# Optimization experiments

Hardware: AMD Instinct MI355X
Metric: run time of the kernel (lower is better)

The kernel has to match this reference:

```python
import jax, jax.numpy as jnp
import numpy as np

N_EMBD = 1024
N_HEAD = 16
B, T = 2, 2048


def setup_inputs() -> dict:
    key = jax.random.key(0)
    ks = jax.random.split(key, 9)
    s = 1.0 / np.sqrt(N_EMBD)
    return {
        "x": jax.random.normal(ks[0], (B, T, N_EMBD), dtype=jnp.float32),
        "Wq": jax.random.normal(ks[1], (N_EMBD, N_EMBD), dtype=jnp.float32) * s,
        "bq": jax.random.normal(ks[2], (N_EMBD,), dtype=jnp.float32) * s,
        "Wk": jax.random.normal(ks[3], (N_EMBD, N_EMBD), dtype=jnp.float32) * s,
        "bk": jax.random.normal(ks[4], (N_EMBD,), dtype=jnp.float32) * s,
        "Wv": jax.random.normal(ks[5], (N_EMBD, N_EMBD), dtype=jnp.float32) * s,
        "bv": jax.random.normal(ks[6], (N_EMBD,), dtype=jnp.float32) * s,
        "Wp": jax.random.normal(ks[7], (N_EMBD, N_EMBD), dtype=jnp.float32) * s,
        "bp": jax.random.normal(ks[8], (N_EMBD,), dtype=jnp.float32) * s,
    }


def reference(x, Wq, bq, Wk, bk, Wv, bv, Wp, bp):
    b, t, c = x.shape
    hd = c // N_HEAD  # head dim
    # torch Linear: x @ W.T + b; reshape to (B, H, T, hd)
    def heads(W, bias):
        return (x @ W.T + bias).reshape(b, t, N_HEAD, hd).transpose(0, 2, 1, 3)
    q, k, v = heads(Wq, bq), heads(Wk, bk), heads(Wv, bv)
    scale = 1.0 / np.sqrt(hd)
    att = jnp.einsum("bhqd,bhkd->bhqk", q, k) * scale  # (B,H,T,T)
    causal = jnp.tril(jnp.ones((t, t), dtype=bool))
    att = jnp.where(causal[None, None], att, -jnp.inf)
    att = jax.nn.softmax(att, axis=-1)
    y = jnp.einsum("bhqk,bhkd->bhqd", att, v)
    y = y.transpose(0, 2, 1, 3).reshape(b, t, c)
    return y @ Wp.T + bp
```

## Files before the change

kernel.cpp:

```cpp
#include <hip/hip_runtime.h>

typedef __bf16 bf16x8 __attribute__((ext_vector_type(8)));
typedef __bf16 bf16x4 __attribute__((ext_vector_type(4)));
typedef float f32x4 __attribute__((ext_vector_type(4)));

#define DEVI __device__ __forceinline__

constexpr int NE = 1024;
constexpr int NH = 16;
constexpr int HD = 64;
constexpr int BB = 2;
constexpr int TT = 2048;
constexpr int MM = BB * TT;

DEVI unsigned short f2bf(float f) {
  union { float f; unsigned u; } v; v.f = f;
  unsigned r = v.u + 0x7FFFu + ((v.u >> 16) & 1u);
  return (unsigned short)(r >> 16);
}

__global__ __launch_bounds__(256) void cvt_bf16(const float* __restrict__ in,
                                                unsigned short* __restrict__ out, int n4) {
  int i = blockIdx.x * blockDim.x + threadIdx.x;
  if (i >= n4) return;
  float4 v = reinterpret_cast<const float4*>(in)[i];
  ushort4 o;
  o.x = f2bf(v.x); o.y = f2bf(v.y); o.z = f2bf(v.z); o.w = f2bf(v.w);
  reinterpret_cast<ushort4*>(out)[i] = o;
}

__global__ __launch_bounds__(256) void cvt_w(const float* __restrict__ q, const float* __restrict__ k,
                                             const float* __restrict__ v, const float* __restrict__ p,
                                             unsigned short* __restrict__ out) {
  int i = blockIdx.x * blockDim.x + threadIdx.x;
  const int seg = i >> 18;
  const float* src = (seg == 0) ? q : (seg == 1) ? k : (seg == 2) ? v : p;
  float4 vv = reinterpret_cast<const float4*>(src)[i & 0x3FFFF];
  ushort4 o;
  o.x = f2bf(vv.x); o.y = f2bf(vv.y); o.z = f2bf(vv.z); o.w = f2bf(vv.w);
  reinterpret_cast<ushort4*>(out)[i] = o;
}

template <int BM, int MODE>
__global__ __launch_bounds__(256, (BM == 128) ? 3 : 2)
void gemm_nt(const unsigned short* __restrict__ A, const unsigned short* __restrict__ Bm,
             const float* __restrict__ b0, const float* __restrict__ b1, const float* __restrict__ b2,
             void* __restrict__ o0, unsigned short* __restrict__ o1, unsigned short* __restrict__ o2,
             int K, int nbx) {
  constexpr int WAVES_N = (BM == 128) ? 2 : 4;
  constexpr int NJ = (BM == 128) ? 4 : 2;
  constexpr int A_LPW = BM / 64;
  __shared__ __align__(16) unsigned short As[3][BM * 32];
  __shared__ __align__(16) unsigned short Bs[3][128 * 32];
  const int tid = threadIdx.x;
  const int wid = tid >> 6;
  const int lane = tid & 63;
  const int l15 = lane & 15, l4 = lane >> 4;

  const int id = blockIdx.x;
  const int chunk = gridDim.x >> 3;
  const int idp = (id & 7) * chunk + (id >> 3);
  const int bx = idp / (gridDim.x / nbx), by = idp % (gridDim.x / nbx);

  const int brow = by * BM;
  const int bcol = bx * 128;
  const int wm = wid / WAVES_N, wn = wid % WAVES_N;
  const int wmoff = wm * 64;
  const int wnoff = wn * (128 / WAVES_N);

  f32x4 acc[4][NJ] = {};

  const int srow = lane >> 2;
  const int sscol = ((lane & 3) ^ ((lane >> 3) & 3)) * 8;

  auto stage = [&](int buf, int t) {
    const int kb = t * 32;
#pragma unroll
    for (int c = 0; c < A_LPW; ++c) {
      const int rb = wid * (BM / 4) + c * 16;
      __builtin_amdgcn_global_load_lds(
          (const __attribute__((address_space(1))) void*)(A + (size_t)(brow + rb + srow) * K + kb + sscol),
          (__attribute__((address_space(3))) void*)&As[buf][rb * 32], 16, 0, 0);
    }
#pragma unroll
    for (int c = 0; c < 2; ++c) {
      const int rb = wid * 32 + c * 16;
      __builtin_amdgcn_global_load_lds(
          (const __attribute__((address_space(1))) void*)(Bm + (size_t)(bcol + rb + srow) * K + kb + sscol),
          (__attribute__((address_space(3))) void*)&Bs[buf][rb * 32], 16, 0, 0);
    }
  };

  const int roff = l15 * 32 + (l4 ^ ((l15 >> 1) & 3)) * 8;

  auto compute = [&](int cb) {
    bf16x8 af[4], bfj[NJ];
#pragma unroll
    for (int i = 0; i < 4; ++i)
      af[i] = *reinterpret_cast<const bf16x8*>(&As[cb][(wmoff + i * 16) * 32 + roff]);
#pragma unroll
    for (int j = 0; j < NJ; ++j)
      bfj[j] = *reinterpret_cast<const bf16x8*>(&Bs[cb][(wnoff + j * 16) * 32 + roff]);
#pragma unroll
    for (int i = 0; i < 4; ++i)
#pragma unroll
      for (int j = 0; j < NJ; ++j)
        acc[i][j] = __builtin_amdgcn_mfma_f32_16x16x32_bf16(af[i], bfj[j], acc[i][j], 0, 0, 0);
  };

  const int NT = K / 32;
  stage(0, 0);
  stage(1, 1);
  int cb = 0, sb = 2;
  for (int t = 0; t + 2 < NT; ++t) {
    stage(sb, t + 2);
    if constexpr (BM == 128) asm volatile("s_waitcnt vmcnt(8)" ::: "memory");
    else                     asm volatile("s_waitcnt vmcnt(6)" ::: "memory");
    asm volatile("s_barrier" ::: "memory");
    compute(cb);
    asm volatile("s_barrier" ::: "memory");
    sb = cb;
    cb = (cb == 2) ? 0 : cb + 1;
  }
  if constexpr (BM == 128) asm volatile("s_waitcnt vmcnt(4)" ::: "memory");
  else                     asm volatile("s_waitcnt vmcnt(3)" ::: "memory");
  asm volatile("s_barrier" ::: "memory");
  compute(cb);
  asm volatile("s_barrier" ::: "memory");
  cb = (cb == 2) ? 0 : cb + 1;
  asm volatile("s_waitcnt vmcnt(0)" ::: "memory");
  asm volatile("s_barrier" ::: "memory");
  compute(cb);

  if (MODE == 0) {
#pragma unroll
    for (int j = 0; j < NJ; ++j) {
      const int col = bcol + wnoff + j * 16 + l15;
      const float bv = b0[col];
#pragma unroll
      for (int i = 0; i < 4; ++i) {
        const int row0 = brow + wmoff + i * 16 + l4 * 4;
#pragma unroll
        for (int r = 0; r < 4; ++r)
          ((float*)o0)[(size_t)(row0 + r) * NE + col] = acc[i][j][r] + bv;
      }
    }
  } else {
    const int seg = bcol >> 10;
    const float* bsel = (seg == 0) ? b0 : (seg == 1) ? b1 : b2;
    unsigned short* qk = (seg == 0) ? (unsigned short*)o0 : o1;
#pragma unroll
    for (int j = 0; j < NJ; ++j) {
      const int col = bcol + wnoff + j * 16 + l15;
      const int dcol = col & 1023;
      const int h = dcol >> 6, d = dcol & 63;
      const float bv = bsel[dcol];
#pragma unroll
      for (int i = 0; i < 4; ++i) {
        const int row0 = brow + wmoff + i * 16 + l4 * 4;
#pragma unroll
        for (int r = 0; r < 4; ++r) {
          const int row = row0 + r;
          const int b = row >> 11, t = row & (TT - 1);
          const unsigned short val = f2bf(acc[i][j][r] + bv);
          if (seg < 2)
            qk[((size_t)((b * NH + h) * TT + t) << 6) + d] = val;
          else
            o2[((size_t)(b * NH + h) * HD + d) * TT + t] = val;
        }
      }
    }
  }
}

__global__ __launch_bounds__(256, 3)
void attn(const unsigned short* __restrict__ Q, const unsigned short* __restrict__ Kk,
          const unsigned short* __restrict__ Vt, unsigned short* __restrict__ Y) {
  __shared__ __align__(16) unsigned short Ks[2][64 * 64];
  __shared__ __align__(16) unsigned short Vs[2][64 * 64];
  __shared__ __align__(16) unsigned short Pw[4][32 * 64];
  const int tid = threadIdx.x, wid = tid >> 6, lane = tid & 63;
  const int l15 = lane & 15, l4 = lane >> 4;

  const int id = blockIdx.x;
  const int v8 = id & 7;
  const int u = id >> 3;
  const int bh = u >> 1;
  const int xt = (u & 1) ? 15 - v8 : v8;

  const int qb0 = xt * 128;
  const int qw = qb0 + wid * 32;
  const unsigned short* Qh = Q + (size_t)bh * TT * HD;
  const unsigned short* Kh = Kk + (size_t)bh * TT * HD;
  const unsigned short* Vh = Vt + (size_t)bh * HD * TT;

  bf16x8 qf[2][2];
#pragma unroll
  for (int qt = 0; qt < 2; ++qt)
#pragma unroll
    for (int ks = 0; ks < 2; ++ks) {
      bf16x8 t = *reinterpret_cast<const bf16x8*>(&Qh[(qw + qt * 16 + l15) * 64 + ks * 32 + l4 * 8]);
#pragma unroll
      for (int e = 0; e < 8; ++e) t[e] = (__bf16)((float)t[e] * 0.18033688011f);
      qf[qt][ks] = t;
    }

  float m_[2] = {-3e38f, -3e38f};
  float l_[2] = {0.f, 0.f};
  f32x4 accO[4][2] = {};

  const int srow8 = lane >> 3;
  const int scol8 = lane & 7;
  const int nkb = 2 * (xt + 1);

  auto stage = [&](int buf, int kb) {
#pragma unroll
    for (int c = 0; c < 2; ++c) {
      const int row = (wid * 2 + c) * 8 + srow8;
      const int sc = (scol8 ^ (row & 7)) * 8;
      __builtin_amdgcn_global_load_lds(
          (const __attribute__((address_space(1))) void*)(Kh + (size_t)(kb + row) * 64 + sc),
          (__attribute__((address_space(3))) void*)&Ks[buf][(wid * 2 + c) * 512], 16, 0, 0);
      __builtin_amdgcn_global_load_lds(
          (const __attribute__((address_space(1))) void*)(Vh + (size_t)row * TT + kb + sc),
          (__attribute__((address_space(3))) void*)&Vs[buf][(wid * 2 + c) * 512], 16, 0, 0);
    }
  };

  stage(0, 0);
  int cur = 0;
  for (int kbi = 0; kbi < nkb; ++kbi) {
    const int kb = kbi * 64;
    __syncthreads();
    if (kbi + 1 < nkb) stage(cur ^ 1, kb + 64);

    if (kb < qw + 32) {
      const bool diag = (kb + 63 > qw);
      const char* ksb = (const char*)Ks[cur];
      const char* vsb = (const char*)Vs[cur];
      char* pwb = (char*)&Pw[wid][0];

      f32x4 z[4][2];
      __builtin_amdgcn_s_setprio(1);
#pragma unroll
      for (int kt = 0; kt < 4; ++kt) {
        const int row = kt * 16 + l15;
        bf16x8 kf0 = *reinterpret_cast<const bf16x8*>(ksb + row * 128 + (((0 + l4) ^ (row & 7)) << 4));
        bf16x8 kf1 = *reinterpret_cast<const bf16x8*>(ksb + row * 128 + (((4 + l4) ^ (row & 7)) << 4));
#pragma unroll
        for (int qt = 0; qt < 2; ++qt) {
          f32x4 zz = {};
          zz = __builtin_amdgcn_mfma_f32_16x16x32_bf16(kf0, qf[qt][0], zz, 0, 0, 0);
          zz = __builtin_amdgcn_mfma_f32_16x16x32_bf16(kf1, qf[qt][1], zz, 0, 0, 0);
          z[kt][qt] = zz;
        }
      }
      __builtin_amdgcn_s_setprio(0);

      if (diag) {
#pragma unroll
        for (int kt = 0; kt < 4; ++kt)
#pragma unroll
          for (int qt = 0; qt < 2; ++qt)
#pragma unroll
            for (int r = 0; r < 4; ++r) {
              const int key = kb + kt * 16 + l4 * 4 + r;
              const int qi = qw + qt * 16 + l15;
              z[kt][qt][r] = (key <= qi) ? z[kt][qt][r] : -3e38f;
            }
      }

#pragma unroll
      for (int qt = 0; qt < 2; ++qt) {
        float tm[8];
#pragma unroll
        for (int i = 0; i < 8; ++i)
          tm[i] = fmaxf(z[(2 * i) >> 2][qt][(2 * i) & 3], z[(2 * i + 1) >> 2][qt][(2 * i + 1) & 3]);
#pragma unroll
        for (int i = 0; i < 4; ++i) tm[i] = fmaxf(tm[i], tm[i + 4]);
        float pm = fmaxf(fmaxf(tm[0], tm[2]), fmaxf(tm[1], tm[3]));
        pm = fmaxf(pm, __shfl_xor(pm, 16, 64));
        pm = fmaxf(pm, __shfl_xor(pm, 32, 64));

        if (!__all(pm <= m_[qt] + 11.5f)) {
          const float mn = fmaxf(m_[qt], pm);
          const float sf = exp2f(m_[qt] - mn);
          m_[qt] = mn;
          l_[qt] *= sf;
#pragma unroll
          for (int dt = 0; dt < 4; ++dt)
#pragma unroll
            for (int r = 0; r < 4; ++r) accO[dt][qt][r] *= sf;
        }

#pragma unroll
        for (int kt = 0; kt < 4; ++kt)
#pragma unroll
          for (int r = 0; r < 4; ++r)
            z[kt][qt][r] = exp2f(z[kt][qt][r] - m_[qt]);
        float ts[8];
#pragma unroll
        for (int i = 0; i < 8; ++i)
          ts[i] = z[(2 * i) >> 2][qt][(2 * i) & 3] + z[(2 * i + 1) >> 2][qt][(2 * i + 1) & 3];
#pragma unroll
        for (int i = 0; i < 4; ++i) ts[i] += ts[i + 4];
        float rs = (ts[0] + ts[2]) + (ts[1] + ts[3]);
        rs += __shfl_xor(rs, 16, 64);
        rs += __shfl_xor(rs, 32, 64);
        l_[qt] += rs;

        const int q = qt * 16 + l15;
#pragma unroll
        for (int kt = 0; kt < 4; ++kt) {
          bf16x4 pk;
#pragma unroll
          for (int r = 0; r < 4; ++r) pk[r] = (__bf16)z[kt][qt][r];
          const int c16 = kt * 2 + (l4 >> 1);
          *reinterpret_cast<bf16x4*>(pwb + q * 128 + ((c16 ^ (q & 7)) << 4) + (l4 & 1) * 8) = pk;
        }
      }

      asm volatile("s_waitcnt lgkmcnt(0)" ::: "memory");
      __builtin_amdgcn_sched_barrier(0);

      __builtin_amdgcn_s_setprio(1);
#pragma unroll
      for (int ks = 0; ks < 2; ++ks) {
        bf16x8 pb[2];
#pragma unroll
        for (int qt = 0; qt < 2; ++qt) {
          const int q = qt * 16 + l15;
          pb[qt] = *reinterpret_cast<const bf16x8*>(pwb + q * 128 + ((((ks << 2) + l4) ^ (q & 7)) << 4));
        }
#pragma unroll
        for (int dt = 0; dt < 4; ++dt) {
          const int row = dt * 16 + l15;
          bf16x8 vf = *reinterpret_cast<const bf16x8*>(vsb + row * 128 + ((((ks << 2) + l4) ^ (row & 7)) << 4));
#pragma unroll
          for (int qt = 0; qt < 2; ++qt)
            accO[dt][qt] = __builtin_amdgcn_mfma_f32_16x16x32_bf16(vf, pb[qt], accO[dt][qt], 0, 0, 0);
        }
      }
      __builtin_amdgcn_s_setprio(0);
    }
    cur ^= 1;
  }

  const int b = bh >> 4, h = bh & 15;
#pragma unroll
  for (int qt = 0; qt < 2; ++qt) {
    const float inv = 1.0f / l_[qt];
    const int q = qw + qt * 16 + l15;
#pragma unroll
    for (int dt = 0; dt < 4; ++dt) {
      bf16x4 o;
#pragma unroll
      for (int r = 0; r < 4; ++r) o[r] = (__bf16)(accO[dt][qt][r] * inv);
      *reinterpret_cast<bf16x4*>(&Y[((size_t)(b * TT + q)) * NE + h * 64 + dt * 16 + l4 * 4]) = o;
    }
  }
}

extern "C" void kernel_launch(void* const* d_in, const int* in_sizes, int n_in,
                              void* d_out, int out_size, void* d_ws, size_t ws_size,
                              hipStream_t stream) {
  const float* x  = (const float*)d_in[0];
  const float* Wq = (const float*)d_in[1];
  const float* bq = (const float*)d_in[2];
  const float* Wk = (const float*)d_in[3];
  const float* bk = (const float*)d_in[4];
  const float* Wv = (const float*)d_in[5];
  const float* bv = (const float*)d_in[6];
  const float* Wp = (const float*)d_in[7];
  const float* bp = (const float*)d_in[8];

  char* ws = (char*)d_ws;
  const size_t MB = 1u << 20;
  unsigned short* xb   = (unsigned short*)(ws + 0 * MB);
  unsigned short* Wqkv = (unsigned short*)(ws + 8 * MB);
  unsigned short* Wpb  = (unsigned short*)(ws + 14 * MB);
  unsigned short* Qb   = (unsigned short*)(ws + 16 * MB);
  unsigned short* Kb   = (unsigned short*)(ws + 24 * MB);
  unsigned short* Vtb  = (unsigned short*)(ws + 32 * MB);
  unsigned short* yb   = (unsigned short*)(ws + 40 * MB);

  cvt_bf16<<<MM * NE / 4 / 256, 256, 0, stream>>>(x, xb, MM * NE / 4);
  cvt_w<<<4 * NE * NE / 4 / 256, 256, 0, stream>>>(Wq, Wk, Wv, Wp, Wqkv);

  gemm_nt<128, 1><<<768, 256, 0, stream>>>(xb, Wqkv, bq, bk, bv, Qb, Kb, Vtb, NE, 24);

  attn<<<512, 256, 0, stream>>>(Qb, Kb, Vtb, yb);

  gemm_nt<64, 0><<<512, 256, 0, stream>>>(yb, Wpb, bp, nullptr, nullptr, d_out, nullptr, nullptr, NE, 8);
}
```

Baseline: 239.6 us.

## Triple-buffer K/V tiles in attention with vmcnt-based waits and reorder block mapping

Moves the attention kernel from double to triple buffering of K/V tiles in LDS. Two tiles are staged ahead, and explicit s_waitcnt vmcnt plus raw s_barrier replace __syncthreads, so global loads overlap more compute. The block-to-(batch-head, q-tile) mapping is also changed so co-scheduled blocks mix different heads and causal lengths. The extra LDS and the lowered occupancy hint (3 to 2 blocks per CU) reduce resident waves, and the hand-counted vmcnt values must match the per-thread load count.

```diff
diff --git a/kernel.cpp b/kernel.cpp
--- a/kernel.cpp
+++ b/kernel.cpp
@@ -173,20 +173,19 @@
   }
 }
 
-__global__ __launch_bounds__(256, 3)
+__global__ __launch_bounds__(256, 2)
 void attn(const unsigned short* __restrict__ Q, const unsigned short* __restrict__ Kk,
           const unsigned short* __restrict__ Vt, unsigned short* __restrict__ Y) {
-  __shared__ __align__(16) unsigned short Ks[2][64 * 64];
-  __shared__ __align__(16) unsigned short Vs[2][64 * 64];
+  __shared__ __align__(16) unsigned short Ks[3][64 * 64];
+  __shared__ __align__(16) unsigned short Vs[3][64 * 64];
   __shared__ __align__(16) unsigned short Pw[4][32 * 64];
   const int tid = threadIdx.x, wid = tid >> 6, lane = tid & 63;
   const int l15 = lane & 15, l4 = lane >> 4;
 
   const int id = blockIdx.x;
-  const int v8 = id & 7;
-  const int u = id >> 3;
-  const int bh = u >> 1;
-  const int xt = (u & 1) ? 15 - v8 : v8;
+  const int j = id & 255, kk = id >> 8;
+  const int bh = (j & 15) + 16 * kk;
+  const int xt = kk ? 15 - (j >> 4) : (j >> 4);
 
   const int qb0 = xt * 128;
   const int qw = qb0 + wid * 32;
@@ -227,124 +226,134 @@
     }
   };
 
+  auto compute_iter = [&](int kbi, int buf) {
+    const int kb = kbi * 64;
+    if (kb >= qw + 32) return;
+    const bool diag = (kb + 63 > qw);
+    const char* ksb = (const char*)Ks[buf];
+    const char* vsb = (const char*)Vs[buf];
+    char* pwb = (char*)&Pw[wid][0];
+
+    f32x4 z[4][2];
+    __builtin_amdgcn_s_setprio(1);
+#pragma unroll
+    for (int kt = 0; kt < 4; ++kt) {
+      const int row = kt * 16 + l15;
+      bf16x8 kf0 = *reinterpret_cast<const bf16x8*>(ksb + row * 128 + (((0 + l4) ^ (row & 7)) << 4));
+      bf16x8 kf1 = *reinterpret_cast<const bf16x8*>(ksb + row * 128 + (((4 + l4) ^ (row & 7)) << 4));
+#pragma unroll
+      for (int qt = 0; qt < 2; ++qt) {
+        f32x4 zz = {};
+        zz = __builtin_amdgcn_mfma_f32_16x16x32_bf16(kf0, qf[qt][0], zz, 0, 0, 0);
+        zz = __builtin_amdgcn_mfma_f32_16x16x32_bf16(kf1, qf[qt][1], zz, 0, 0, 0);
+        z[kt][qt] = zz;
+      }
+    }
+    __builtin_amdgcn_s_setprio(0);
+
+    if (diag) {
+#pragma unroll
+      for (int kt = 0; kt < 4; ++kt)
+#pragma unroll
+        for (int qt = 0; qt < 2; ++qt)
+#pragma unroll
+          for (int r = 0; r < 4; ++r) {
+            const int key = kb + kt * 16 + l4 * 4 + r;
+            const int qi = qw + qt * 16 + l15;
+            z[kt][qt][r] = (key <= qi) ? z[kt][qt][r] : -3e38f;
+          }
+    }
+
+#pragma unroll
+    for (int qt = 0; qt < 2; ++qt) {
+      float tm[8];
+#pragma unroll
+      for (int i = 0; i < 8; ++i)
+        tm[i] = fmaxf(z[(2 * i) >> 2][qt][(2 * i) & 3], z[(2 * i + 1) >> 2][qt][(2 * i + 1) & 3]);
+#pragma unroll
+      for (int i = 0; i < 4; ++i) tm[i] = fmaxf(tm[i], tm[i + 4]);
+      float pm = fmaxf(fmaxf(tm[0], tm[2]), fmaxf(tm[1], tm[3]));
+      pm = fmaxf(pm, __shfl_xor(pm, 16, 64));
+      pm = fmaxf(pm, __shfl_xor(pm, 32, 64));
+
+      if (!__all(pm <= m_[qt] + 11.5f)) {
+        const float mn = fmaxf(m_[qt], pm);
+        const float sf = exp2f(m_[qt] - mn);
+        m_[qt] = mn;
+        l_[qt] *= sf;
+#pragma unroll
+        for (int dt = 0; dt < 4; ++dt)
+#pragma unroll
+          for (int r = 0; r < 4; ++r) accO[dt][qt][r] *= sf;
+      }
+
+#pragma unroll
+      for (int kt = 0; kt < 4; ++kt)
+#pragma unroll
+        for (int r = 0; r < 4; ++r)
+          z[kt][qt][r] = exp2f(z[kt][qt][r] - m_[qt]);
+      float ts[8];
+#pragma unroll
+      for (int i = 0; i < 8; ++i)
+        ts[i] = z[(2 * i) >> 2][qt][(2 * i) & 3] + z[(2 * i + 1) >> 2][qt][(2 * i + 1) & 3];
+#pragma unroll
+      for (int i = 0; i < 4; ++i) ts[i] += ts[i + 4];
+      float rs = (ts[0] + ts[2]) + (ts[1] + ts[3]);
+      rs += __shfl_xor(rs, 16, 64);
+      rs += __shfl_xor(rs, 32, 64);
+      l_[qt] += rs;
+
+      const int q = qt * 16 + l15;
+#pragma unroll
+      for (int kt = 0; kt < 4; ++kt) {
+        bf16x4 pk;
+#pragma unroll
+        for (int r = 0; r < 4; ++r) pk[r] = (__bf16)z[kt][qt][r];
+        const int c16 = kt * 2 + (l4 >> 1);
+        *reinterpret_cast<bf16x4*>(pwb + q * 128 + ((c16 ^ (q & 7)) << 4) + (l4 & 1) * 8) = pk;
+      }
+    }
+
+    asm volatile("s_waitcnt lgkmcnt(0)" ::: "memory");
+    __builtin_amdgcn_sched_barrier(0);
+
+    __builtin_amdgcn_s_setprio(1);
+#pragma unroll
+    for (int ks = 0; ks < 2; ++ks) {
+      bf16x8 pb[2];
+#pragma unroll
+      for (int qt = 0; qt < 2; ++qt) {
+        const int q = qt * 16 + l15;
+        pb[qt] = *reinterpret_cast<const bf16x8*>(pwb + q * 128 + ((((ks << 2) + l4) ^ (q & 7)) << 4));
+      }
+#pragma unroll
+      for (int dt = 0; dt < 4; ++dt) {
+        const int row = dt * 16 + l15;
+        bf16x8 vf = *reinterpret_cast<const bf16x8*>(vsb + row * 128 + ((((ks << 2) + l4) ^ (row & 7)) << 4));
+#pragma unroll
+        for (int qt = 0; qt < 2; ++qt)
+          accO[dt][qt] = __builtin_amdgcn_mfma_f32_16x16x32_bf16(vf, pb[qt], accO[dt][qt], 0, 0, 0);
+      }
+    }
+    __builtin_amdgcn_s_setprio(0);
+  };
+
   stage(0, 0);
-  int cur = 0;
-  for (int kbi = 0; kbi < nkb; ++kbi) {
-    const int kb = kbi * 64;
-    __syncthreads();
-    if (kbi + 1 < nkb) stage(cur ^ 1, kb + 64);
-
-    if (kb < qw + 32) {
-      const bool diag = (kb + 63 > qw);
-      const char* ksb = (const char*)Ks[cur];
-      const char* vsb = (const char*)Vs[cur];
-      char* pwb = (char*)&Pw[wid][0];
-
-      f32x4 z[4][2];
-      __builtin_amdgcn_s_setprio(1);
-#pragma unroll
-      for (int kt = 0; kt < 4; ++kt) {
-        const int row = kt * 16 + l15;
-        bf16x8 kf0 = *reinterpret_cast<const bf16x8*>(ksb + row * 128 + (((0 + l4) ^ (row & 7)) << 4));
-        bf16x8 kf1 = *reinterpret_cast<const bf16x8*>(ksb + row * 128 + (((4 + l4) ^ (row & 7)) << 4));
-#pragma unroll
-        for (int qt = 0; qt < 2; ++qt) {
-          f32x4 zz = {};
-          zz = __builtin_amdgcn_mfma_f32_16x16x32_bf16(kf0, qf[qt][0], zz, 0, 0, 0);
-          zz = __builtin_amdgcn_mfma_f32_16x16x32_bf16(kf1, qf[qt][1], zz, 0, 0, 0);
-          z[kt][qt] = zz;
-        }
-      }
-      __builtin_amdgcn_s_setprio(0);
-
-      if (diag) {
-#pragma unroll
-        for (int kt = 0; kt < 4; ++kt)
-#pragma unroll
-          for (int qt = 0; qt < 2; ++qt)
-#pragma unroll
-            for (int r = 0; r < 4; ++r) {
-              const int key = kb + kt * 16 + l4 * 4 + r;
-              const int qi = qw + qt * 16 + l15;
-              z[kt][qt][r] = (key <= qi) ? z[kt][qt][r] : -3e38f;
-            }
-      }
-
-#pragma unroll
-      for (int qt = 0; qt < 2; ++qt) {
-        float tm[8];
-#pragma unroll
-        for (int i = 0; i < 8; ++i)
-          tm[i] = fmaxf(z[(2 * i) >> 2][qt][(2 * i) & 3], z[(2 * i + 1) >> 2][qt][(2 * i + 1) & 3]);
-#pragma unroll
-        for (int i = 0; i < 4; ++i) tm[i] = fmaxf(tm[i], tm[i + 4]);
-        float pm = fmaxf(fmaxf(tm[0], tm[2]), fmaxf(tm[1], tm[3]));
-        pm = fmaxf(pm, __shfl_xor(pm, 16, 64));
-        pm = fmaxf(pm, __shfl_xor(pm, 32, 64));
-
-        if (!__all(pm <= m_[qt] + 11.5f)) {
-          const float mn = fmaxf(m_[qt], pm);
-          const float sf = exp2f(m_[qt] - mn);
-          m_[qt] = mn;
-          l_[qt] *= sf;
-#pragma unroll
-          for (int dt = 0; dt < 4; ++dt)
-#pragma unroll
-            for (int r = 0; r < 4; ++r) accO[dt][qt][r] *= sf;
-        }
-
-#pragma unroll
-        for (int kt = 0; kt < 4; ++kt)
-#pragma unroll
-          for (int r = 0; r < 4; ++r)
-            z[kt][qt][r] = exp2f(z[kt][qt][r] - m_[qt]);
-        float ts[8];
-#pragma unroll
-        for (int i = 0; i < 8; ++i)
-          ts[i] = z[(2 * i) >> 2][qt][(2 * i) & 3] + z[(2 * i + 1) >> 2][qt][(2 * i + 1) & 3];
-#pragma unroll
-        for (int i = 0; i < 4; ++i) ts[i] += ts[i + 4];
-        float rs = (ts[0] + ts[2]) + (ts[1] + ts[3]);
-        rs += __shfl_xor(rs, 16, 64);
-        rs += __shfl_xor(rs, 32, 64);
-        l_[qt] += rs;
-
-        const int q = qt * 16 + l15;
-#pragma unroll
-        for (int kt = 0; kt < 4; ++kt) {
-          bf16x4 pk;
-#pragma unroll
-          for (int r = 0; r < 4; ++r) pk[r] = (__bf16)z[kt][qt][r];
-          const int c16 = kt * 2 + (l4 >> 1);
-          *reinterpret_cast<bf16x4*>(pwb + q * 128 + ((c16 ^ (q & 7)) << 4) + (l4 & 1) * 8) = pk;
-        }
-      }
-
-      asm volatile("s_waitcnt lgkmcnt(0)" ::: "memory");
-      __builtin_amdgcn_sched_barrier(0);
-
-      __builtin_amdgcn_s_setprio(1);
-#pragma unroll
-      for (int ks = 0; ks < 2; ++ks) {
-        bf16x8 pb[2];
-#pragma unroll
-        for (int qt = 0; qt < 2; ++qt) {
-          const int q = qt * 16 + l15;
-          pb[qt] = *reinterpret_cast<const bf16x8*>(pwb + q * 128 + ((((ks << 2) + l4) ^ (q & 7)) << 4));
-        }
-#pragma unroll
-        for (int dt = 0; dt < 4; ++dt) {
-          const int row = dt * 16 + l15;
-          bf16x8 vf = *reinterpret_cast<const bf16x8*>(vsb + row * 128 + ((((ks << 2) + l4) ^ (row & 7)) << 4));
-#pragma unroll
-          for (int qt = 0; qt < 2; ++qt)
-            accO[dt][qt] = __builtin_amdgcn_mfma_f32_16x16x32_bf16(vf, pb[qt], accO[dt][qt], 0, 0, 0);
-        }
-      }
-      __builtin_amdgcn_s_setprio(0);
-    }
-    cur ^= 1;
+  stage(1, 64);
+  for (int t = 0; t + 2 < nkb; ++t) {
+    stage((t + 2) % 3, (t + 2) * 64);
+    asm volatile("s_waitcnt vmcnt(8)" ::: "memory");
+    asm volatile("s_barrier" ::: "memory");
+    compute_iter(t, t % 3);
+    asm volatile("s_barrier" ::: "memory");
   }
+  asm volatile("s_waitcnt vmcnt(4)" ::: "memory");
+  asm volatile("s_barrier" ::: "memory");
+  compute_iter(nkb - 2, (nkb - 2) % 3);
+  asm volatile("s_barrier" ::: "memory");
+  asm volatile("s_waitcnt vmcnt(0)" ::: "memory");
+  asm volatile("s_barrier" ::: "memory");
+  compute_iter(nkb - 1, (nkb - 1) % 3);
 
   const int b = bh >> 4, h = bh & 15;
 #pragma unroll
```

New measurement: 223.6 us. -6.7%, faster.

## Widen attention key tile to 128 and remap blocks across heads

Applied to the files above, without the earlier changes.

The attention kernel now processes 128 keys per iteration instead of 64, with larger double-buffered K/V shared tiles and a new XOR swizzle for the wider V tile. This halves the loop trip count, syncs and online-softmax rescale checks per key. It also removes the per-wave skip branch, since the last tile is always the diagonal one. Block-index mapping changes so the first half of the grid walks query tiles ascending and the second half descending across heads, to balance causal work. The cost is doubled shared memory and more live registers, so launch bounds drop to 2 blocks per CU, reducing occupancy.

```diff
diff --git a/kernel.cpp b/kernel.cpp
--- a/kernel.cpp
+++ b/kernel.cpp
@@ -173,23 +173,22 @@
   }
 }
 
-__global__ __launch_bounds__(256, 3)
+__global__ __launch_bounds__(256, 2)
 void attn(const unsigned short* __restrict__ Q, const unsigned short* __restrict__ Kk,
           const unsigned short* __restrict__ Vt, unsigned short* __restrict__ Y) {
-  __shared__ __align__(16) unsigned short Ks[2][64 * 64];
-  __shared__ __align__(16) unsigned short Vs[2][64 * 64];
+  __shared__ __align__(16) unsigned short Ks[2][128 * 64];
+  __shared__ __align__(16) unsigned short Vs[2][64 * 128];
   __shared__ __align__(16) unsigned short Pw[4][32 * 64];
   const int tid = threadIdx.x, wid = tid >> 6, lane = tid & 63;
   const int l15 = lane & 15, l4 = lane >> 4;
 
   const int id = blockIdx.x;
-  const int v8 = id & 7;
-  const int u = id >> 3;
-  const int bh = u >> 1;
-  const int xt = (u & 1) ? 15 - v8 : v8;
-
-  const int qb0 = xt * 128;
-  const int qw = qb0 + wid * 32;
+  const int j = id & 255, kk = id >> 8;
+  const int bh = (j & 15) + 16 * kk;
+  const int xt = kk ? 15 - (j >> 4) : (j >> 4);
+
+  const int qw = xt * 128 + wid * 32;
+  const int nkb = xt + 1;
   const unsigned short* Qh = Q + (size_t)bh * TT * HD;
   const unsigned short* Kh = Kk + (size_t)bh * TT * HD;
   const unsigned short* Vh = Vt + (size_t)bh * HD * TT;
@@ -209,139 +208,151 @@
   float l_[2] = {0.f, 0.f};
   f32x4 accO[4][2] = {};
 
-  const int srow8 = lane >> 3;
-  const int scol8 = lane & 7;
-  const int nkb = 2 * (xt + 1);
-
   auto stage = [&](int buf, int kb) {
 #pragma unroll
-    for (int c = 0; c < 2; ++c) {
-      const int row = (wid * 2 + c) * 8 + srow8;
-      const int sc = (scol8 ^ (row & 7)) * 8;
+    for (int c = 0; c < 4; ++c) {
+      const int row = wid * 32 + c * 8 + (lane >> 3);
+      const int sc = ((lane & 7) ^ (lane >> 3)) * 8;
       __builtin_amdgcn_global_load_lds(
           (const __attribute__((address_space(1))) void*)(Kh + (size_t)(kb + row) * 64 + sc),
-          (__attribute__((address_space(3))) void*)&Ks[buf][(wid * 2 + c) * 512], 16, 0, 0);
+          (__attribute__((address_space(3))) void*)&Ks[buf][(wid * 32 + c * 8) * 64], 16, 0, 0);
+    }
+#pragma unroll
+    for (int c = 0; c < 4; ++c) {
+      const int row = wid * 16 + c * 4 + (lane >> 4);
+      const int sc = ((lane & 15) ^ (c * 4 + (lane >> 4))) * 8;
       __builtin_amdgcn_global_load_lds(
           (const __attribute__((address_space(1))) void*)(Vh + (size_t)row * TT + kb + sc),
-          (__attribute__((address_space(3))) void*)&Vs[buf][(wid * 2 + c) * 512], 16, 0, 0);
+          (__attribute__((address_space(3))) void*)&Vs[buf][(wid * 16 + c * 4) * 128], 16, 0, 0);
     }
   };
 
   stage(0, 0);
   int cur = 0;
   for (int kbi = 0; kbi < nkb; ++kbi) {
-    const int kb = kbi * 64;
+    const int kb = kbi * 128;
     __syncthreads();
-    if (kbi + 1 < nkb) stage(cur ^ 1, kb + 64);
-
-    if (kb < qw + 32) {
-      const bool diag = (kb + 63 > qw);
-      const char* ksb = (const char*)Ks[cur];
-      const char* vsb = (const char*)Vs[cur];
-      char* pwb = (char*)&Pw[wid][0];
-
-      f32x4 z[4][2];
-      __builtin_amdgcn_s_setprio(1);
-#pragma unroll
-      for (int kt = 0; kt < 4; ++kt) {
-        const int row = kt * 16 + l15;
-        bf16x8 kf0 = *reinterpret_cast<const bf16x8*>(ksb + row * 128 + (((0 + l4) ^ (row & 7)) << 4));
-        bf16x8 kf1 = *reinterpret_cast<const bf16x8*>(ksb + row * 128 + (((4 + l4) ^ (row & 7)) << 4));
-#pragma unroll
-        for (int qt = 0; qt < 2; ++qt) {
-          f32x4 zz = {};
-          zz = __builtin_amdgcn_mfma_f32_16x16x32_bf16(kf0, qf[qt][0], zz, 0, 0, 0);
-          zz = __builtin_amdgcn_mfma_f32_16x16x32_bf16(kf1, qf[qt][1], zz, 0, 0, 0);
-          z[kt][qt] = zz;
-        }
-      }
-      __builtin_amdgcn_s_setprio(0);
-
-      if (diag) {
-#pragma unroll
-        for (int kt = 0; kt < 4; ++kt)
-#pragma unroll
-          for (int qt = 0; qt < 2; ++qt)
-#pragma unroll
-            for (int r = 0; r < 4; ++r) {
-              const int key = kb + kt * 16 + l4 * 4 + r;
-              const int qi = qw + qt * 16 + l15;
-              z[kt][qt][r] = (key <= qi) ? z[kt][qt][r] : -3e38f;
-            }
-      }
-
+    if (kbi + 1 < nkb) stage(cur ^ 1, kb + 128);
+
+    const bool diag = (kbi == nkb - 1);
+    const char* ksb = (const char*)Ks[cur];
+    const char* vsb = (const char*)Vs[cur];
+    char* pwb = (char*)&Pw[wid][0];
+
+    f32x4 z[8][2];
+    __builtin_amdgcn_s_setprio(1);
+#pragma unroll
+    for (int kt = 0; kt < 8; ++kt) {
+      const int row = kt * 16 + l15;
+      const char* base = ksb + row * 128;
+      bf16x8 kf0 = *reinterpret_cast<const bf16x8*>(base + (((0 + l4) ^ (l15 & 7)) << 4));
+      bf16x8 kf1 = *reinterpret_cast<const bf16x8*>(base + (((4 + l4) ^ (l15 & 7)) << 4));
 #pragma unroll
       for (int qt = 0; qt < 2; ++qt) {
-        float tm[8];
-#pragma unroll
-        for (int i = 0; i < 8; ++i)
-          tm[i] = fmaxf(z[(2 * i) >> 2][qt][(2 * i) & 3], z[(2 * i + 1) >> 2][qt][(2 * i + 1) & 3]);
-#pragma unroll
-        for (int i = 0; i < 4; ++i) tm[i] = fmaxf(tm[i], tm[i + 4]);
-        float pm = fmaxf(fmaxf(tm[0], tm[2]), fmaxf(tm[1], tm[3]));
-        pm = fmaxf(pm, __shfl_xor(pm, 16, 64));
-        pm = fmaxf(pm, __shfl_xor(pm, 32, 64));
-
-        if (!__all(pm <= m_[qt] + 11.5f)) {
-          const float mn = fmaxf(m_[qt], pm);
-          const float sf = exp2f(m_[qt] - mn);
-          m_[qt] = mn;
-          l_[qt] *= sf;
-#pragma unroll
-          for (int dt = 0; dt < 4; ++dt)
-#pragma unroll
-            for (int r = 0; r < 4; ++r) accO[dt][qt][r] *= sf;
-        }
-
-#pragma unroll
-        for (int kt = 0; kt < 4; ++kt)
-#pragma unroll
-          for (int r = 0; r < 4; ++r)
-            z[kt][qt][r] = exp2f(z[kt][qt][r] - m_[qt]);
-        float ts[8];
-#pragma unroll
-        for (int i = 0; i < 8; ++i)
-          ts[i] = z[(2 * i) >> 2][qt][(2 * i) & 3] + z[(2 * i + 1) >> 2][qt][(2 * i + 1) & 3];
-#pragma unroll
-        for (int i = 0; i < 4; ++i) ts[i] += ts[i + 4];
-        float rs = (ts[0] + ts[2]) + (ts[1] + ts[3]);
-        rs += __shfl_xor(rs, 16, 64);
-        rs += __shfl_xor(rs, 32, 64);
-        l_[qt] += rs;
-
+        f32x4 zz = {};
+        zz = __builtin_amdgcn_mfma_f32_16x16x32_bf16(kf0, qf[qt][0], zz, 0, 0, 0);
+        zz = __builtin_amdgcn_mfma_f32_16x16x32_bf16(kf1, qf[qt][1], zz, 0, 0, 0);
+        z[kt][qt] = zz;
+      }
+    }
+    __builtin_amdgcn_s_setprio(0);
+
+    if (diag) {
+#pragma unroll
+      for (int kt = 0; kt < 8; ++kt)
+#pragma unroll
+        for (int qt = 0; qt < 2; ++qt)
+#pragma unroll
+          for (int r = 0; r < 4; ++r) {
+            const int key = kb + kt * 16 + l4 * 4 + r;
+            const int qi = qw + qt * 16 + l15;
+            z[kt][qt][r] = (key <= qi) ? z[kt][qt][r] : -3e38f;
+          }
+    }
+
+#pragma unroll
+    for (int qt = 0; qt < 2; ++qt) {
+      float tm[16];
+#pragma unroll
+      for (int i = 0; i < 16; ++i)
+        tm[i] = fmaxf(z[(2 * i) >> 2][qt][(2 * i) & 3], z[(2 * i + 1) >> 2][qt][(2 * i + 1) & 3]);
+#pragma unroll
+      for (int i = 0; i < 8; ++i) tm[i] = fmaxf(tm[i], tm[i + 8]);
+#pragma unroll
+      for (int i = 0; i < 4; ++i) tm[i] = fmaxf(tm[i], tm[i + 4]);
+      float pm = fmaxf(fmaxf(tm[0], tm[2]), fmaxf(tm[1], tm[3]));
+      pm = fmaxf(pm, __shfl_xor(pm, 16, 64));
+      pm = fmaxf(pm, __shfl_xor(pm, 32, 64));
+
+      if (!__all(pm <= m_[qt] + 11.5f)) {
+        const float mn = fmaxf(m_[qt], pm);
+        const float sf = exp2f(m_[qt] - mn);
+        m_[qt] = mn;
+        l_[qt] *= sf;
+#pragma unroll
+        for (int dt = 0; dt < 4; ++dt)
+#pragma unroll
+          for (int r = 0; r < 4; ++r) accO[dt][qt][r] *= sf;
+      }
+
+#pragma unroll
+      for (int kt = 0; kt < 8; ++kt)
+#pragma unroll
+        for (int r = 0; r < 4; ++r)
+          z[kt][qt][r] = exp2f(z[kt][qt][r] - m_[qt]);
+      float ts[16];
+#pragma unroll
+      for (int i = 0; i < 16; ++i)
+        ts[i] = z[(2 * i) >> 2][qt][(2 * i) & 3] + z[(2 * i + 1) >> 2][qt][(2 * i + 1) & 3];
+#pragma unroll
+      for (int i = 0; i < 8; ++i) ts[i] += ts[i + 8];
+#pragma unroll
+      for (int i = 0; i < 4; ++i) ts[i] += ts[i + 4];
+      float rs = (ts[0] + ts[2]) + (ts[1] + ts[3]);
+      rs += __shfl_xor(rs, 16, 64);
+      rs += __shfl_xor(rs, 32, 64);
+      l_[qt] += rs;
+    }
+
+#pragma unroll
+    for (int h = 0; h < 2; ++h) {
+#pragma unroll
+      for (int qt = 0; qt < 2; ++qt) {
         const int q = qt * 16 + l15;
 #pragma unroll
-        for (int kt = 0; kt < 4; ++kt) {
+        for (int k4 = 0; k4 < 4; ++k4) {
+          const int kt = h * 4 + k4;
           bf16x4 pk;
 #pragma unroll
           for (int r = 0; r < 4; ++r) pk[r] = (__bf16)z[kt][qt][r];
-          const int c16 = kt * 2 + (l4 >> 1);
+          const int c16 = k4 * 2 + (l4 >> 1);
           *reinterpret_cast<bf16x4*>(pwb + q * 128 + ((c16 ^ (q & 7)) << 4) + (l4 & 1) * 8) = pk;
         }
       }
-
       asm volatile("s_waitcnt lgkmcnt(0)" ::: "memory");
       __builtin_amdgcn_sched_barrier(0);
 
       __builtin_amdgcn_s_setprio(1);
 #pragma unroll
-      for (int ks = 0; ks < 2; ++ks) {
+      for (int ks2 = 0; ks2 < 2; ++ks2) {
         bf16x8 pb[2];
 #pragma unroll
         for (int qt = 0; qt < 2; ++qt) {
           const int q = qt * 16 + l15;
-          pb[qt] = *reinterpret_cast<const bf16x8*>(pwb + q * 128 + ((((ks << 2) + l4) ^ (q & 7)) << 4));
+          pb[qt] = *reinterpret_cast<const bf16x8*>(pwb + q * 128 + ((((ks2 << 2) + l4) ^ (q & 7)) << 4));
         }
 #pragma unroll
         for (int dt = 0; dt < 4; ++dt) {
           const int row = dt * 16 + l15;
-          bf16x8 vf = *reinterpret_cast<const bf16x8*>(vsb + row * 128 + ((((ks << 2) + l4) ^ (row & 7)) << 4));
+          bf16x8 vf = *reinterpret_cast<const bf16x8*>(
+              vsb + row * 256 + ((((h * 2 + ks2) * 4 + l4) ^ l15) << 4));
 #pragma unroll
           for (int qt = 0; qt < 2; ++qt)
             accO[dt][qt] = __builtin_amdgcn_mfma_f32_16x16x32_bf16(vf, pb[qt], accO[dt][qt], 0, 0, 0);
         }
       }
       __builtin_amdgcn_s_setprio(0);
+      __builtin_amdgcn_sched_barrier(0);
     }
     cur ^= 1;
   }
```

Result: faster. 214.9 us (-10.3%).
